# Kernel optimization log

Hardware: AMD Instinct MI355X
Metric: run time of the kernel (lower is better)

## Reference

```python
import jax, jax.numpy as jnp
import numpy as np

N = 10000
E = 640000
F = 128      # in_dim
H = 4        # heads
Dh = 32      # head_dim = ceil(128/4)
INNER = H * Dh   # 128 == out_dim -> W_out is Identity
OUT = 128
SCALE = 1.0 / np.sqrt(float(Dh))
LN_EPS = 1e-5


def setup_inputs() -> dict:
    key = jax.random.key(0)
    ks = jax.random.split(key, 8)
    s = 1.0 / np.sqrt(F)
    nodes = jax.random.normal(ks[0], (N, F), dtype=jnp.float32)
    edge_index = jax.random.randint(ks[1], (2, E), 0, N, dtype=jnp.int32)
    W_Q = jax.random.uniform(ks[2], (F, INNER), jnp.float32, -s, s)
    W_K = jax.random.uniform(ks[3], (F, INNER), jnp.float32, -s, s)
    W_V = jax.random.uniform(ks[4], (F, INNER), jnp.float32, -s, s)
    W_res = jax.random.uniform(ks[5], (F, OUT), jnp.float32, -s, s)
    b_res = jax.random.uniform(ks[6], (OUT,), jnp.float32, -s, s)
    gamma = jnp.ones((OUT,), jnp.float32)
    beta = jnp.zeros((OUT,), jnp.float32)
    return {"nodes": nodes, "W_Q": W_Q, "W_K": W_K, "W_V": W_V,
            "W_res": W_res, "b_res": b_res, "gamma": gamma, "beta": beta,
            "edge_index": edge_index}


def reference(nodes, W_Q, W_K, W_V, W_res, b_res, gamma, beta, edge_index):
    n = nodes.shape[0]
    src = edge_index[0]
    dst = edge_index[1]
    # node-level projections, split into heads: [N, H, Dh]
    Q = (nodes @ W_Q).reshape(n, H, Dh)
    K = (nodes @ W_K).reshape(n, H, Dh)
    V = (nodes @ W_V).reshape(n, H, Dh)
    # per-edge gathers: q from dst, k/v from src
    q = Q[dst]          # [E, H, Dh]
    k = K[src]
    v = V[src]
    score = jnp.sum(q * k, axis=-1) * SCALE      # [E, H]
    # segment softmax over dst
    mx = jax.ops.segment_max(score, dst, num_segments=n)   # [N, H]
    mx = jnp.where(jnp.isfinite(mx), mx, 0.0)               # guard empty segments
    ex = jnp.exp(score - mx[dst])                           # [E, H]
    sm = jax.ops.segment_sum(ex, dst, num_segments=n)       # [N, H]
    alpha = ex / (sm[dst] + 1e-12)                          # [E, H]
    # scatter-aggregate weighted values
    agg = jax.ops.segment_sum(alpha[:, :, None] * v, dst, num_segments=n)  # [N, H, Dh]
    H_cat = agg.reshape(n, INNER)                # W_out is Identity (inner == out)
    H_out = H_cat + nodes @ W_res + b_res        # residual projection
    # LayerNorm(out_dim)
    mu = jnp.mean(H_out, axis=-1, keepdims=True)
    var = jnp.mean(jnp.square(H_out - mu), axis=-1, keepdims=True)
    x_hat = (H_out - mu) * jax.lax.rsqrt(var + LN_EPS)
    return gamma * x_hat + beta
```

## Files before the change

kernel.cpp:

```cpp
#include <hip/hip_runtime.h>
#include <math.h>

#define FDIM 128
#define NP 64
#define NMAX 10240
static constexpr float SC2 = 0.17677669529663687f * 1.4426950408889634f;
static constexpr float LN_EPS = 1e-5f;

typedef __attribute__((ext_vector_type(8))) short bf16x8;
typedef __attribute__((ext_vector_type(4))) float f32x4;

__device__ __forceinline__ unsigned short f2bf(float f) {
    unsigned u = __float_as_uint(f);
    unsigned r = u + 0x7FFFu + ((u >> 16) & 1u);
    return (unsigned short)(r >> 16);
}

__global__ __launch_bounds__(256) void prep_kernel(
    const float* __restrict__ Wq, const float* __restrict__ Wk,
    const float* __restrict__ Wv, const float* __restrict__ Wr,
    unsigned short* __restrict__ Wt)
{
    const int tid = threadIdx.x;
    const int t = blockIdx.x;
    const int wiW = t >> 2, q = t & 3;
    const float* __restrict__ W = (wiW == 0) ? Wq : (wiW == 1) ? Wk : (wiW == 2) ? Wv : Wr;
    const int c = q * 32 + (tid >> 3);
    const int k0 = (tid & 7) * 16;
    unsigned short* dp = &Wt[(size_t)wiW * 16384 + c * 128 + k0];
    #pragma unroll
    for (int kk = 0; kk < 16; ++kk)
        dp[kk] = f2bf(W[(k0 + kk) * FDIM + c]);
}

__global__ __launch_bounds__(256) void gemm_hist_kernel(
    const float* __restrict__ nodes,
    const unsigned short* __restrict__ Wt,
    const float* __restrict__ br,
    unsigned short* __restrict__ Qu, unsigned short* __restrict__ KVu,
    float* __restrict__ Rb, int N,
    const int* __restrict__ dst, int* __restrict__ bh,
    int* __restrict__ rank, int E, int C)
{
    __shared__ __align__(16) char smem[52224];
    const int tid = threadIdx.x;
    const int wi = blockIdx.y;

    if (wi == 0) {
        const int p = blockIdx.x;
        if (p >= NP) return;
        int* h = (int*)smem;
        for (int i = tid; i < N; i += 256) h[i] = 0;
        __syncthreads();
        const int lo = p * C;
        const int hi = min(lo + C, E);
        const int n = hi - lo;
        if (n > 0) {
            if (((lo | E) & 3) == 0) {
                const int4* d4 = (const int4*)(dst + lo);
                int4* r4p = (int4*)(rank + lo);
                const int n4 = n >> 2;
                for (int i = tid; i < n4; i += 256) {
                    int4 d = d4[i];
                    int4 r;
                    r.x = atomicAdd(&h[d.x], 1);
                    r.y = atomicAdd(&h[d.y], 1);
                    r.z = atomicAdd(&h[d.z], 1);
                    r.w = atomicAdd(&h[d.w], 1);
                    r4p[i] = r;
                }
                for (int i = lo + (n4 << 2) + tid; i < hi; i += 256)
                    rank[i] = atomicAdd(&h[dst[i]], 1);
            } else {
                for (int i = lo + tid; i < hi; i += 256)
                    rank[i] = atomicAdd(&h[dst[i]], 1);
            }
        }
        __syncthreads();
        for (int i = tid; i < N; i += 256) bh[p * N + i] = h[i];
        return;
    }

    const int gw = wi - 1;
    const int row0 = blockIdx.x * 64;
    unsigned short (*As)[136] = (unsigned short(*)[136])smem;
    unsigned short (*Ws)[136] = (unsigned short(*)[136])(smem + 64 * 272);

    #pragma unroll
    for (int i = 0; i < 8; ++i) {
        const int idx = tid + i * 256;
        const int r = idx >> 5, c4 = idx & 31;
        const int gr = row0 + r;
        float4 v = make_float4(0.f, 0.f, 0.f, 0.f);
        if (gr < N) v = *reinterpret_cast<const float4*>(&nodes[(size_t)gr * FDIM + c4 * 4]);
        ushort4 o;
        o.x = f2bf(v.x); o.y = f2bf(v.y); o.z = f2bf(v.z); o.w = f2bf(v.w);
        *reinterpret_cast<ushort4*>(&As[r][c4 * 4]) = o;
    }
    const unsigned short* Wg = &Wt[(size_t)gw * 16384];
    #pragma unroll
    for (int i = 0; i < 8; ++i) {
        const int idx = tid + i * 256;
        const int r = idx >> 4, ch = idx & 15;
        const uint4 v = *reinterpret_cast<const uint4*>(&Wg[r * 128 + ch * 8]);
        *reinterpret_cast<uint4*>(&Ws[r][ch * 8]) = v;
    }
    __syncthreads();

    const int w = tid >> 6;
    const int l = tid & 63;
    const int lr = l & 15;
    const int lh = l >> 4;

    f32x4 acc[8];
    #pragma unroll
    for (int ct = 0; ct < 8; ++ct) acc[ct] = (f32x4){0.f, 0.f, 0.f, 0.f};

    #pragma unroll
    for (int kc = 0; kc < 4; ++kc) {
        const bf16x8 a = *reinterpret_cast<const bf16x8*>(&As[w * 16 + lr][kc * 32 + lh * 8]);
        #pragma unroll
        for (int ct = 0; ct < 8; ++ct) {
            const bf16x8 bb = *reinterpret_cast<const bf16x8*>(&Ws[ct * 16 + lr][kc * 32 + lh * 8]);
            acc[ct] = __builtin_amdgcn_mfma_f32_16x16x32_bf16(a, bb, acc[ct], 0, 0, 0);
        }
    }

    const int rbase = row0 + w * 16 + lh * 4;
    #pragma unroll
    for (int ct = 0; ct < 8; ++ct) {
        const int col = ct * 16 + lr;
        float bc = 0.f;
        if (gw == 3) bc = br[col];
        #pragma unroll
        for (int r = 0; r < 4; ++r) {
            const int row = rbase + r;
            if (row >= N) continue;
            const float val = acc[ct][r];
            if (gw == 0)      Qu[(size_t)row * 128 + col] = f2bf(val);
            else if (gw == 1) KVu[(size_t)row * 256 + col] = f2bf(val);
            else if (gw == 2) KVu[(size_t)row * 256 + 128 + col] = f2bf(val);
            else              Rb[(size_t)row * 128 + col] = val + bc;
        }
    }
}

__global__ __launch_bounds__(256) void deg_kernel(
    const int* __restrict__ bh, int* __restrict__ deg, int N)
{
    const int d = blockIdx.x * 256 + threadIdx.x;
    if (d < N) {
        int s = 0;
        #pragma unroll
        for (int p = 0; p < NP; ++p) s += bh[p * N + d];
        deg[d] = s;
    }
}

__global__ __launch_bounds__(1024) void scan_kernel(
    const int* __restrict__ deg, int* __restrict__ rowptr, int N)
{
    __shared__ int tot[NMAX];
    __shared__ int wsum[16];
    const int tid = threadIdx.x;
    const int lane = tid & 63;
    const int wid = tid >> 6;

    for (int d = tid; d < N; d += 1024) tot[d] = deg[d];
    __syncthreads();

    const int CH = (N + 1023) / 1024;
    const int b = tid * CH;
    const int e = min(b + CH, N);
    int s = 0;
    for (int i = b; i < e; ++i) s += tot[i];

    int incl = s;
    #pragma unroll
    for (int off = 1; off < 64; off <<= 1) {
        int t = __shfl_up(incl, off);
        if (lane >= off) incl += t;
    }
    if (lane == 63) wsum[wid] = incl;
    __syncthreads();
    if (wid == 0) {
        int v = (lane < 16) ? wsum[lane] : 0;
        #pragma unroll
        for (int off = 1; off < 16; off <<= 1) {
            int t = __shfl_up(v, off);
            if (lane >= off) v += t;
        }
        if (lane < 16) wsum[lane] = v;
    }
    __syncthreads();
    const int wbase = (wid > 0) ? wsum[wid - 1] : 0;
    int run = wbase + incl - s;
    for (int i = b; i < e; ++i) {
        const int t = tot[i];
        rowptr[i] = run;
        run += t;
    }
    if (tid == 1023) rowptr[N] = wsum[15];
}

__global__ __launch_bounds__(256) void base_kernel(
    int* __restrict__ bh, const int* __restrict__ rowptr, int N)
{
    const int d = blockIdx.x * 256 + threadIdx.x;
    if (d < N) {
        int c = rowptr[d];
        #pragma unroll
        for (int p = 0; p < NP; ++p) {
            const int cnt = bh[p * N + d];
            bh[p * N + d] = c;
            c += cnt;
        }
    }
}

__global__ __launch_bounds__(256) void scatter_kernel(
    const int* __restrict__ src, const int* __restrict__ dst,
    const int* __restrict__ rank, const int* __restrict__ base,
    int* __restrict__ ssrc, int N, int E, int C)
{
    const int p = blockIdx.x >> 3;
    const int sub = blockIdx.x & 7;
    const int CS = C >> 3;
    const int lo = p * C + sub * CS;
    const int hi = min(lo + CS, E);
    const int n = hi - lo;
    if (n <= 0) return;
    const int* bp = &base[p * N];

    if (((lo | E) & 3) == 0) {
        const int4* s4 = (const int4*)(src + lo);
        const int4* d4 = (const int4*)(dst + lo);
        const int4* r4 = (const int4*)(rank + lo);
        const int n4 = n >> 2;
        for (int i = threadIdx.x; i < n4; i += 256) {
            const int4 s = s4[i];
            const int4 d = d4[i];
            const int4 r = r4[i];
            ssrc[bp[d.x] + r.x] = s.x;
            ssrc[bp[d.y] + r.y] = s.y;
            ssrc[bp[d.z] + r.z] = s.z;
            ssrc[bp[d.w] + r.w] = s.w;
        }
        for (int i = lo + (n4 << 2) + threadIdx.x; i < hi; i += 256)
            ssrc[bp[dst[i]] + rank[i]] = src[i];
    } else {
        for (int i = lo + threadIdx.x; i < hi; i += 256)
            ssrc[bp[dst[i]] + rank[i]] = src[i];
    }
}

__global__ __launch_bounds__(256) void agg_kernel(
    const unsigned short* __restrict__ Qu, const unsigned short* __restrict__ KVu,
    const float* __restrict__ Rb,
    const int* __restrict__ rowptr, const int* __restrict__ ssrc,
    const float* __restrict__ gamma, const float* __restrict__ beta,
    float* __restrict__ out, int N)
{
    const int wave = threadIdx.x >> 6;
    const int lane = threadIdx.x & 63;
    const int qtr = lane >> 4;
    const int lq = lane & 15;
    const int n = blockIdx.x * 16 + wave * 4 + qtr;
    if (n >= N) return;
    const int d0 = lq * 8;

    const uint4 qu = *reinterpret_cast<const uint4*>(&Qu[(size_t)n * 128 + d0]);
    const float qf0 = __uint_as_float(qu.x << 16), qf1 = __uint_as_float(qu.x & 0xFFFF0000u);
    const float qf2 = __uint_as_float(qu.y << 16), qf3 = __uint_as_float(qu.y & 0xFFFF0000u);
    const float qf4 = __uint_as_float(qu.z << 16), qf5 = __uint_as_float(qu.z & 0xFFFF0000u);
    const float qf6 = __uint_as_float(qu.w << 16), qf7 = __uint_as_float(qu.w & 0xFFFF0000u);

    const int beg = rowptr[n];
    const int end = rowptr[n + 1];

    float4 A0a = make_float4(0.f, 0.f, 0.f, 0.f), A0b = A0a;
    float4 A1a = A0a, A1b = A0a, A2a = A0a, A2b = A0a, A3a = A0a, A3b = A0a;
    float L0 = 0.f, L1 = 0.f, L2 = 0.f, L3 = 0.f;

#define GATHER(S, NK, NV)                                                     \
    {                                                                         \
        const unsigned short* bp = &KVu[(size_t)(S) * 256 + d0];              \
        NK = *reinterpret_cast<const uint4*>(bp);                             \
        NV = *reinterpret_cast<const uint4*>(bp + 128);                       \
    }
#define STEP(KU, VU, Aa, Ab, L)                                               \
    {                                                                         \
        const float k0 = __uint_as_float((KU).x << 16), k1 = __uint_as_float((KU).x & 0xFFFF0000u); \
        const float k2 = __uint_as_float((KU).y << 16), k3 = __uint_as_float((KU).y & 0xFFFF0000u); \
        const float k4 = __uint_as_float((KU).z << 16), k5 = __uint_as_float((KU).z & 0xFFFF0000u); \
        const float k6 = __uint_as_float((KU).w << 16), k7 = __uint_as_float((KU).w & 0xFFFF0000u); \
        float p = qf0 * k0 + qf1 * k1 + qf2 * k2 + qf3 * k3                   \
                + qf4 * k4 + qf5 * k5 + qf6 * k6 + qf7 * k7;                  \
        p += __shfl_xor(p, 1);                                                \
        p += __shfl_xor(p, 2);                                                \
        const float e1 = exp2f(p * SC2);                                      \
        const float v0 = __uint_as_float((VU).x << 16), v1 = __uint_as_float((VU).x & 0xFFFF0000u); \
        const float v2 = __uint_as_float((VU).y << 16), v3 = __uint_as_float((VU).y & 0xFFFF0000u); \
        const float v4 = __uint_as_float((VU).z << 16), v5 = __uint_as_float((VU).z & 0xFFFF0000u); \
        const float v6 = __uint_as_float((VU).w << 16), v7 = __uint_as_float((VU).w & 0xFFFF0000u); \
        Aa.x += e1 * v0; Aa.y += e1 * v1; Aa.z += e1 * v2; Aa.w += e1 * v3;   \
        Ab.x += e1 * v4; Ab.y += e1 * v5; Ab.z += e1 * v6; Ab.w += e1 * v7;   \
        L += e1;                                                              \
    }

    uint4 nk0, nv0, nk1, nv1, nk2, nv2, nk3, nv3;
    int j = beg;
    const int nb = (end - beg) >> 2;
    if (nb > 0) {
        int c0i = ssrc[j], c1i = ssrc[j + 1], c2i = ssrc[j + 2], c3i = ssrc[j + 3];
        GATHER(c0i, nk0, nv0); GATHER(c1i, nk1, nv1);
        GATHER(c2i, nk2, nv2); GATHER(c3i, nk3, nv3);
        int x0 = ssrc[j + 4], x1 = ssrc[j + 5], x2 = ssrc[j + 6], x3 = ssrc[j + 7];
        for (int bi = 1; bi < nb; ++bi) {
            const uint4 ck0 = nk0, cv0 = nv0, ck1 = nk1, cv1 = nv1;
            const uint4 ck2 = nk2, cv2 = nv2, ck3 = nk3, cv3 = nv3;
            c0i = x0; c1i = x1; c2i = x2; c3i = x3;
            const int nbase = j + (bi + 1) * 4;
            x0 = ssrc[nbase]; x1 = ssrc[nbase + 1];
            x2 = ssrc[nbase + 2]; x3 = ssrc[nbase + 3];
            GATHER(c0i, nk0, nv0); GATHER(c1i, nk1, nv1);
            GATHER(c2i, nk2, nv2); GATHER(c3i, nk3, nv3);
            STEP(ck0, cv0, A0a, A0b, L0);
            STEP(ck1, cv1, A1a, A1b, L1);
            STEP(ck2, cv2, A2a, A2b, L2);
            STEP(ck3, cv3, A3a, A3b, L3);
        }
        STEP(nk0, nv0, A0a, A0b, L0);
        STEP(nk1, nv1, A1a, A1b, L1);
        STEP(nk2, nv2, A2a, A2b, L2);
        STEP(nk3, nv3, A3a, A3b, L3);
        j = beg + nb * 4;
    }
    for (; j < end; ++j) {
        const int s0 = ssrc[j];
        uint4 k0u, v0u;
        GATHER(s0, k0u, v0u);
        STEP(k0u, v0u, A0a, A0b, L0);
    }
#undef GATHER
#undef STEP

    const float L = (L0 + L1) + (L2 + L3);
    const float inv = 1.f / (L + 1e-12f);
    const float4 ra = *reinterpret_cast<const float4*>(&Rb[(size_t)n * 128 + d0]);
    const float4 rb = *reinterpret_cast<const float4*>(&Rb[(size_t)n * 128 + d0 + 4]);
    float xa0 = ((A0a.x + A1a.x) + (A2a.x + A3a.x)) * inv + ra.x;
    float xa1 = ((A0a.y + A1a.y) + (A2a.y + A3a.y)) * inv + ra.y;
    float xa2 = ((A0a.z + A1a.z) + (A2a.z + A3a.z)) * inv + ra.z;
    float xa3 = ((A0a.w + A1a.w) + (A2a.w + A3a.w)) * inv + ra.w;
    float xb0 = ((A0b.x + A1b.x) + (A2b.x + A3b.x)) * inv + rb.x;
    float xb1 = ((A0b.y + A1b.y) + (A2b.y + A3b.y)) * inv + rb.y;
    float xb2 = ((A0b.z + A1b.z) + (A2b.z + A3b.z)) * inv + rb.z;
    float xb3 = ((A0b.w + A1b.w) + (A2b.w + A3b.w)) * inv + rb.w;

    float s1v = (xa0 + xa1 + xa2 + xa3) + (xb0 + xb1 + xb2 + xb3);
    float s2v = xa0 * xa0 + xa1 * xa1 + xa2 * xa2 + xa3 * xa3
              + xb0 * xb0 + xb1 * xb1 + xb2 * xb2 + xb3 * xb3;
    #pragma unroll
    for (int off = 8; off; off >>= 1) {
        s1v += __shfl_xor(s1v, off);
        s2v += __shfl_xor(s2v, off);
    }
    const float mu = s1v * (1.f / 128.f);
    float var = s2v * (1.f / 128.f) - mu * mu;
    var = fmaxf(var, 0.f);
    const float rs = rsqrtf(var + LN_EPS);

    const float4 ga = *reinterpret_cast<const float4*>(&gamma[d0]);
    const float4 gb = *reinterpret_cast<const float4*>(&gamma[d0 + 4]);
    const float4 ba = *reinterpret_cast<const float4*>(&beta[d0]);
    const float4 bb = *reinterpret_cast<const float4*>(&beta[d0 + 4]);
    float4 oa, ob;
    oa.x = ga.x * (xa0 - mu) * rs + ba.x;
    oa.y = ga.y * (xa1 - mu) * rs + ba.y;
    oa.z = ga.z * (xa2 - mu) * rs + ba.z;
    oa.w = ga.w * (xa3 - mu) * rs + ba.w;
    ob.x = gb.x * (xb0 - mu) * rs + bb.x;
    ob.y = gb.y * (xb1 - mu) * rs + bb.y;
    ob.z = gb.z * (xb2 - mu) * rs + bb.z;
    ob.w = gb.w * (xb3 - mu) * rs + bb.w;
    *reinterpret_cast<float4*>(&out[(size_t)n * 128 + d0]) = oa;
    *reinterpret_cast<float4*>(&out[(size_t)n * 128 + d0 + 4]) = ob;
}

extern "C" void kernel_launch(void* const* d_in, const int* in_sizes, int n_in,
                              void* d_out, int out_size, void* d_ws, size_t ws_size,
                              hipStream_t stream)
{
    const float* nodes = (const float*)d_in[0];
    const float* W_Q   = (const float*)d_in[1];
    const float* W_K   = (const float*)d_in[2];
    const float* W_V   = (const float*)d_in[3];
    const float* W_res = (const float*)d_in[4];
    const float* b_res = (const float*)d_in[5];
    const float* gamma = (const float*)d_in[6];
    const float* beta  = (const float*)d_in[7];
    const int*   eidx  = (const int*)d_in[8];

    const int N = in_sizes[0] / FDIM;
    const int E = in_sizes[8] / 2;
    const int* src = eidx;
    const int* dst = eidx + E;

    float* out = (float*)d_out;

    unsigned short* KVu = (unsigned short*)d_ws;
    unsigned short* Qu  = KVu + (size_t)N * 256;
    unsigned short* Wt  = Qu + (size_t)N * 128;
    float* Rb   = (float*)(Wt + 4 * 16384);
    int* bh     = (int*)(Rb + (size_t)N * 128);
    int* rowptr = bh + (size_t)NP * N;
    int* deg    = rowptr + (N + 1);
    int* rank   = deg + N;
    int* ssrc   = rank + E;

    const int C = (((E + NP - 1) / NP) + 31) & ~31;
    const int nG = (N + 63) / 64;
    const int nB = (N + 255) / 256;

    prep_kernel<<<16, 256, 0, stream>>>(W_Q, W_K, W_V, W_res, Wt);

    dim3 ggrid(nG, 5);
    gemm_hist_kernel<<<ggrid, 256, 0, stream>>>(nodes, Wt, b_res,
                                                Qu, KVu, Rb, N, dst, bh, rank, E, C);
    deg_kernel<<<nB, 256, 0, stream>>>(bh, deg, N);
    scan_kernel<<<1, 1024, 0, stream>>>(deg, rowptr, N);
    base_kernel<<<nB, 256, 0, stream>>>(bh, rowptr, N);
    scatter_kernel<<<NP * 8, 256, 0, stream>>>(src, dst, rank, bh, ssrc, N, E, C);
    agg_kernel<<<(N + 15) / 16, 256, 0, stream>>>(Qu, KVu, Rb, rowptr, ssrc,
                                                  gamma, beta, out, N);
}
```

Baseline: 88.52 us.

## Fuse weight prep into GEMM, merge degree/base passes, triple-buffer agg gathers

Each GEMM block now transposes and converts the fp32 weights to bf16 in shared memory itself, so the separate prep kernel goes away. The per-partition offset computation moves into the degree kernel as relative offsets, and the scatter adds rowptr itself, so base_kernel and one launch are removed. The aggregation loop now keeps three groups of four edges in flight instead of one prefetched group, to hide gather latency. The cost is redundant weight conversion in every GEMM block, strided transposed LDS writes, and higher register pressure in agg_kernel.

Result: slower. 115.7 us (+30.7%).

```diff
diff --git a/kernel.cpp b/kernel.cpp
--- a/kernel.cpp
+++ b/kernel.cpp
@@ -16,26 +16,10 @@
     return (unsigned short)(r >> 16);
 }
 
-__global__ __launch_bounds__(256) void prep_kernel(
+__global__ __launch_bounds__(256) void gemm_hist_kernel(
+    const float* __restrict__ nodes,
     const float* __restrict__ Wq, const float* __restrict__ Wk,
     const float* __restrict__ Wv, const float* __restrict__ Wr,
-    unsigned short* __restrict__ Wt)
-{
-    const int tid = threadIdx.x;
-    const int t = blockIdx.x;
-    const int wiW = t >> 2, q = t & 3;
-    const float* __restrict__ W = (wiW == 0) ? Wq : (wiW == 1) ? Wk : (wiW == 2) ? Wv : Wr;
-    const int c = q * 32 + (tid >> 3);
-    const int k0 = (tid & 7) * 16;
-    unsigned short* dp = &Wt[(size_t)wiW * 16384 + c * 128 + k0];
-    #pragma unroll
-    for (int kk = 0; kk < 16; ++kk)
-        dp[kk] = f2bf(W[(k0 + kk) * FDIM + c]);
-}
-
-__global__ __launch_bounds__(256) void gemm_hist_kernel(
-    const float* __restrict__ nodes,
-    const unsigned short* __restrict__ Wt,
     const float* __restrict__ br,
     unsigned short* __restrict__ Qu, unsigned short* __restrict__ KVu,
     float* __restrict__ Rb, int N,
@@ -97,13 +81,17 @@
         o.x = f2bf(v.x); o.y = f2bf(v.y); o.z = f2bf(v.z); o.w = f2bf(v.w);
         *reinterpret_cast<ushort4*>(&As[r][c4 * 4]) = o;
     }
-    const unsigned short* Wg = &Wt[(size_t)gw * 16384];
-    #pragma unroll
-    for (int i = 0; i < 8; ++i) {
+    const float* __restrict__ Wg = (gw == 0) ? Wq : (gw == 1) ? Wk : (gw == 2) ? Wv : Wr;
+    #pragma unroll
+    for (int i = 0; i < 16; ++i) {
         const int idx = tid + i * 256;
-        const int r = idx >> 4, ch = idx & 15;
-        const uint4 v = *reinterpret_cast<const uint4*>(&Wg[r * 128 + ch * 8]);
-        *reinterpret_cast<uint4*>(&Ws[r][ch * 8]) = v;
+        const int kr = idx >> 5;
+        const int c0i = (idx & 31) * 4;
+        const float4 v = *reinterpret_cast<const float4*>(&Wg[kr * FDIM + c0i]);
+        Ws[c0i + 0][kr] = f2bf(v.x);
+        Ws[c0i + 1][kr] = f2bf(v.y);
+        Ws[c0i + 2][kr] = f2bf(v.z);
+        Ws[c0i + 3][kr] = f2bf(v.w);
     }
     __syncthreads();
 
@@ -145,15 +133,19 @@
     }
 }
 
-__global__ __launch_bounds__(256) void deg_kernel(
-    const int* __restrict__ bh, int* __restrict__ deg, int N)
+__global__ __launch_bounds__(256) void degrel_kernel(
+    int* __restrict__ bh, int* __restrict__ deg, int N)
 {
     const int d = blockIdx.x * 256 + threadIdx.x;
     if (d < N) {
-        int s = 0;
+        int c = 0;
         #pragma unroll
-        for (int p = 0; p < NP; ++p) s += bh[p * N + d];
-        deg[d] = s;
+        for (int p = 0; p < NP; ++p) {
+            const int cnt = bh[p * N + d];
+            bh[p * N + d] = c;
+            c += cnt;
+        }
+        deg[d] = c;
     }
 }
 
@@ -203,25 +195,11 @@
     if (tid == 1023) rowptr[N] = wsum[15];
 }
 
-__global__ __launch_bounds__(256) void base_kernel(
-    int* __restrict__ bh, const int* __restrict__ rowptr, int N)
-{
-    const int d = blockIdx.x * 256 + threadIdx.x;
-    if (d < N) {
-        int c = rowptr[d];
-        #pragma unroll
-        for (int p = 0; p < NP; ++p) {
-            const int cnt = bh[p * N + d];
-            bh[p * N + d] = c;
-            c += cnt;
-        }
-    }
-}
-
 __global__ __launch_bounds__(256) void scatter_kernel(
     const int* __restrict__ src, const int* __restrict__ dst,
-    const int* __restrict__ rank, const int* __restrict__ base,
-    int* __restrict__ ssrc, int N, int E, int C)
+    const int* __restrict__ rank, const int* __restrict__ rel,
+    const int* __restrict__ rowptr, int* __restrict__ ssrc,
+    int N, int E, int C)
 {
     const int p = blockIdx.x >> 3;
     const int sub = blockIdx.x & 7;
@@ -230,7 +208,7 @@
     const int hi = min(lo + CS, E);
     const int n = hi - lo;
     if (n <= 0) return;
-    const int* bp = &base[p * N];
+    const int* rp = &rel[p * N];
 
     if (((lo | E) & 3) == 0) {
         const int4* s4 = (const int4*)(src + lo);
@@ -241,16 +219,16 @@
             const int4 s = s4[i];
             const int4 d = d4[i];
             const int4 r = r4[i];
-            ssrc[bp[d.x] + r.x] = s.x;
-            ssrc[bp[d.y] + r.y] = s.y;
-            ssrc[bp[d.z] + r.z] = s.z;
-            ssrc[bp[d.w] + r.w] = s.w;
+            ssrc[rowptr[d.x] + rp[d.x] + r.x] = s.x;
+            ssrc[rowptr[d.y] + rp[d.y] + r.y] = s.y;
+            ssrc[rowptr[d.z] + rp[d.z] + r.z] = s.z;
+            ssrc[rowptr[d.w] + rp[d.w] + r.w] = s.w;
         }
         for (int i = lo + (n4 << 2) + threadIdx.x; i < hi; i += 256)
-            ssrc[bp[dst[i]] + rank[i]] = src[i];
+            ssrc[rowptr[dst[i]] + rp[dst[i]] + rank[i]] = src[i];
     } else {
         for (int i = lo + threadIdx.x; i < hi; i += 256)
-            ssrc[bp[dst[i]] + rank[i]] = src[i];
+            ssrc[rowptr[dst[i]] + rp[dst[i]] + rank[i]] = src[i];
     }
 }
 
@@ -282,12 +260,6 @@
     float4 A1a = A0a, A1b = A0a, A2a = A0a, A2b = A0a, A3a = A0a, A3b = A0a;
     float L0 = 0.f, L1 = 0.f, L2 = 0.f, L3 = 0.f;
 
-#define GATHER(S, NK, NV)                                                     \
-    {                                                                         \
-        const unsigned short* bp = &KVu[(size_t)(S) * 256 + d0];              \
-        NK = *reinterpret_cast<const uint4*>(bp);                             \
-        NV = *reinterpret_cast<const uint4*>(bp + 128);                       \
-    }
 #define STEP(KU, VU, Aa, Ab, L)                                               \
     {                                                                         \
         const float k0 = __uint_as_float((KU).x << 16), k1 = __uint_as_float((KU).x & 0xFFFF0000u); \
@@ -307,42 +279,67 @@
         Ab.x += e1 * v4; Ab.y += e1 * v5; Ab.z += e1 * v6; Ab.w += e1 * v7;   \
         L += e1;                                                              \
     }
-
-    uint4 nk0, nv0, nk1, nv1, nk2, nv2, nk3, nv3;
+#define GATH(P, JJ)                                                           \
+    {                                                                         \
+        const int t0 = ssrc[JJ], t1 = ssrc[(JJ) + 1];                         \
+        const int t2 = ssrc[(JJ) + 2], t3 = ssrc[(JJ) + 3];                   \
+        const unsigned short* p0 = &KVu[(size_t)t0 * 256 + d0];               \
+        const unsigned short* p1 = &KVu[(size_t)t1 * 256 + d0];               \
+        const unsigned short* p2 = &KVu[(size_t)t2 * 256 + d0];               \
+        const unsigned short* p3 = &KVu[(size_t)t3 * 256 + d0];               \
+        P##K0 = *reinterpret_cast<const uint4*>(p0);                          \
+        P##V0 = *reinterpret_cast<const uint4*>(p0 + 128);                    \
+        P##K1 = *reinterpret_cast<const uint4*>(p1);                          \
+        P##V1 = *reinterpret_cast<const uint4*>(p1 + 128);                    \
+        P##K2 = *reinterpret_cast<const uint4*>(p2);                          \
+        P##V2 = *reinterpret_cast<const uint4*>(p2 + 128);                    \
+        P##K3 = *reinterpret_cast<const uint4*>(p3);                          \
+        P##V3 = *reinterpret_cast<const uint4*>(p3 + 128);                    \
+    }
+#define STEP4(P)                                                              \
+    STEP(P##K0, P##V0, A0a, A0b, L0);                                         \
+    STEP(P##K1, P##V1, A1a, A1b, L1);                                         \
+    STEP(P##K2, P##V2, A2a, A2b, L2);                                         \
+    STEP(P##K3, P##V3, A3a, A3b, L3);
+
+    uint4 aK0, aV0, aK1, aV1, aK2, aV2, aK3, aV3;
+    uint4 bK0, bV0, bK1, bV1, bK2, bV2, bK3, bV3;
+    uint4 cK0, cV0, cK1, cV1, cK2, cV2, cK3, cV3;
+
     int j = beg;
     const int nb = (end - beg) >> 2;
-    if (nb > 0) {
-        int c0i = ssrc[j], c1i = ssrc[j + 1], c2i = ssrc[j + 2], c3i = ssrc[j + 3];
-        GATHER(c0i, nk0, nv0); GATHER(c1i, nk1, nv1);
-        GATHER(c2i, nk2, nv2); GATHER(c3i, nk3, nv3);
-        int x0 = ssrc[j + 4], x1 = ssrc[j + 5], x2 = ssrc[j + 6], x3 = ssrc[j + 7];
-        for (int bi = 1; bi < nb; ++bi) {
-            const uint4 ck0 = nk0, cv0 = nv0, ck1 = nk1, cv1 = nv1;
-            const uint4 ck2 = nk2, cv2 = nv2, ck3 = nk3, cv3 = nv3;
-            c0i = x0; c1i = x1; c2i = x2; c3i = x3;
-            const int nbase = j + (bi + 1) * 4;
-            x0 = ssrc[nbase]; x1 = ssrc[nbase + 1];
-            x2 = ssrc[nbase + 2]; x3 = ssrc[nbase + 3];
-            GATHER(c0i, nk0, nv0); GATHER(c1i, nk1, nv1);
-            GATHER(c2i, nk2, nv2); GATHER(c3i, nk3, nv3);
-            STEP(ck0, cv0, A0a, A0b, L0);
-            STEP(ck1, cv1, A1a, A1b, L1);
-            STEP(ck2, cv2, A2a, A2b, L2);
-            STEP(ck3, cv3, A3a, A3b, L3);
-        }
-        STEP(nk0, nv0, A0a, A0b, L0);
-        STEP(nk1, nv1, A1a, A1b, L1);
-        STEP(nk2, nv2, A2a, A2b, L2);
-        STEP(nk3, nv3, A3a, A3b, L3);
+    if (nb >= 3) {
+        GATH(a, j); GATH(b, j + 4); GATH(c, j + 8);
+        int bi = 0;
+        for (; bi + 5 < nb; bi += 3) {
+            STEP4(a); GATH(a, j + (bi + 3) * 4);
+            STEP4(b); GATH(b, j + (bi + 4) * 4);
+            STEP4(c); GATH(c, j + (bi + 5) * 4);
+        }
+        STEP4(a);
+        if (bi + 3 < nb) GATH(a, j + (bi + 3) * 4);
+        STEP4(b);
+        if (bi + 4 < nb) GATH(b, j + (bi + 4) * 4);
+        STEP4(c);
+        if (bi + 3 < nb) { STEP4(a); }
+        if (bi + 4 < nb) { STEP4(b); }
+        j = beg + nb * 4;
+    } else if (nb > 0) {
+        GATH(a, j);
+        if (nb == 2) GATH(b, j + 4);
+        STEP4(a);
+        if (nb == 2) { STEP4(b); }
         j = beg + nb * 4;
     }
     for (; j < end; ++j) {
         const int s0 = ssrc[j];
-        uint4 k0u, v0u;
-        GATHER(s0, k0u, v0u);
+        const unsigned short* bp = &KVu[(size_t)s0 * 256 + d0];
+        const uint4 k0u = *reinterpret_cast<const uint4*>(bp);
+        const uint4 v0u = *reinterpret_cast<const uint4*>(bp + 128);
         STEP(k0u, v0u, A0a, A0b, L0);
     }
-#undef GATHER
+#undef STEP4
+#undef GATH
 #undef STEP
 
     const float L = (L0 + L1) + (L2 + L3);
@@ -411,8 +408,7 @@
 
     unsigned short* KVu = (unsigned short*)d_ws;
     unsigned short* Qu  = KVu + (size_t)N * 256;
-    unsigned short* Wt  = Qu + (size_t)N * 128;
-    float* Rb   = (float*)(Wt + 4 * 16384);
+    float* Rb   = (float*)(Qu + (size_t)N * 128);
     int* bh     = (int*)(Rb + (size_t)N * 128);
     int* rowptr = bh + (size_t)NP * N;
     int* deg    = rowptr + (N + 1);
@@ -423,15 +419,12 @@
     const int nG = (N + 63) / 64;
     const int nB = (N + 255) / 256;
 
-    prep_kernel<<<16, 256, 0, stream>>>(W_Q, W_K, W_V, W_res, Wt);
-
     dim3 ggrid(nG, 5);
-    gemm_hist_kernel<<<ggrid, 256, 0, stream>>>(nodes, Wt, b_res,
+    gemm_hist_kernel<<<ggrid, 256, 0, stream>>>(nodes, W_Q, W_K, W_V, W_res, b_res,
                                                 Qu, KVu, Rb, N, dst, bh, rank, E, C);
-    deg_kernel<<<nB, 256, 0, stream>>>(bh, deg, N);
+    degrel_kernel<<<nB, 256, 0, stream>>>(bh, deg, N);
     scan_kernel<<<1, 1024, 0, stream>>>(deg, rowptr, N);
-    base_kernel<<<nB, 256, 0, stream>>>(bh, rowptr, N);
-    scatter_kernel<<<NP * 8, 256, 0, stream>>>(src, dst, rank, bh, ssrc, N, E, C);
+    scatter_kernel<<<NP * 8, 256, 0, stream>>>(src, dst, rank, bh, rowptr, ssrc, N, E, C);
     agg_kernel<<<(N + 15) / 16, 256, 0, stream>>>(Qu, KVu, Rb, rowptr, ssrc,
                                                   gamma, beta, out, N);
 }
```

## Fold weight prep into GEMM and merge base offsets into degree pass

Applied to the files above, without the earlier changes.

Drops the separate weight-transpose/bf16 prep kernel: each GEMM block now reads fp32 weights directly, converts them to bf16 and transposes them into shared memory. It also folds the per-partition base computation into the degree kernel as relative offsets, so the scatter adds rowptr at write time and the base kernel launch goes away. This removes two launches and one full pass over the histogram. In exchange, every GEMM block does redundant weight conversion with scattered 2-byte LDS stores, and the scatter does an extra rowptr gather per edge.

Result: slower. 95.80 us (+8.2%).

```diff
diff --git a/kernel.cpp b/kernel.cpp
--- a/kernel.cpp
+++ b/kernel.cpp
@@ -16,26 +16,10 @@
     return (unsigned short)(r >> 16);
 }
 
-__global__ __launch_bounds__(256) void prep_kernel(
+__global__ __launch_bounds__(256) void gemm_hist_kernel(
+    const float* __restrict__ nodes,
     const float* __restrict__ Wq, const float* __restrict__ Wk,
     const float* __restrict__ Wv, const float* __restrict__ Wr,
-    unsigned short* __restrict__ Wt)
-{
-    const int tid = threadIdx.x;
-    const int t = blockIdx.x;
-    const int wiW = t >> 2, q = t & 3;
-    const float* __restrict__ W = (wiW == 0) ? Wq : (wiW == 1) ? Wk : (wiW == 2) ? Wv : Wr;
-    const int c = q * 32 + (tid >> 3);
-    const int k0 = (tid & 7) * 16;
-    unsigned short* dp = &Wt[(size_t)wiW * 16384 + c * 128 + k0];
-    #pragma unroll
-    for (int kk = 0; kk < 16; ++kk)
-        dp[kk] = f2bf(W[(k0 + kk) * FDIM + c]);
-}
-
-__global__ __launch_bounds__(256) void gemm_hist_kernel(
-    const float* __restrict__ nodes,
-    const unsigned short* __restrict__ Wt,
     const float* __restrict__ br,
     unsigned short* __restrict__ Qu, unsigned short* __restrict__ KVu,
     float* __restrict__ Rb, int N,
@@ -97,13 +81,17 @@
         o.x = f2bf(v.x); o.y = f2bf(v.y); o.z = f2bf(v.z); o.w = f2bf(v.w);
         *reinterpret_cast<ushort4*>(&As[r][c4 * 4]) = o;
     }
-    const unsigned short* Wg = &Wt[(size_t)gw * 16384];
-    #pragma unroll
-    for (int i = 0; i < 8; ++i) {
+    const float* __restrict__ Wg = (gw == 0) ? Wq : (gw == 1) ? Wk : (gw == 2) ? Wv : Wr;
+    #pragma unroll
+    for (int i = 0; i < 16; ++i) {
         const int idx = tid + i * 256;
-        const int r = idx >> 4, ch = idx & 15;
-        const uint4 v = *reinterpret_cast<const uint4*>(&Wg[r * 128 + ch * 8]);
-        *reinterpret_cast<uint4*>(&Ws[r][ch * 8]) = v;
+        const int kr = idx >> 5;
+        const int c0i = (idx & 31) * 4;
+        const float4 v = *reinterpret_cast<const float4*>(&Wg[kr * FDIM + c0i]);
+        Ws[c0i + 0][kr] = f2bf(v.x);
+        Ws[c0i + 1][kr] = f2bf(v.y);
+        Ws[c0i + 2][kr] = f2bf(v.z);
+        Ws[c0i + 3][kr] = f2bf(v.w);
     }
     __syncthreads();
 
@@ -145,15 +133,19 @@
     }
 }
 
-__global__ __launch_bounds__(256) void deg_kernel(
-    const int* __restrict__ bh, int* __restrict__ deg, int N)
+__global__ __launch_bounds__(256) void degrel_kernel(
+    int* __restrict__ bh, int* __restrict__ deg, int N)
 {
     const int d = blockIdx.x * 256 + threadIdx.x;
     if (d < N) {
-        int s = 0;
+        int c = 0;
         #pragma unroll
-        for (int p = 0; p < NP; ++p) s += bh[p * N + d];
-        deg[d] = s;
+        for (int p = 0; p < NP; ++p) {
+            const int cnt = bh[p * N + d];
+            bh[p * N + d] = c;
+            c += cnt;
+        }
+        deg[d] = c;
     }
 }
 
@@ -203,25 +195,11 @@
     if (tid == 1023) rowptr[N] = wsum[15];
 }
 
-__global__ __launch_bounds__(256) void base_kernel(
-    int* __restrict__ bh, const int* __restrict__ rowptr, int N)
-{
-    const int d = blockIdx.x * 256 + threadIdx.x;
-    if (d < N) {
-        int c = rowptr[d];
-        #pragma unroll
-        for (int p = 0; p < NP; ++p) {
-            const int cnt = bh[p * N + d];
-            bh[p * N + d] = c;
-            c += cnt;
-        }
-    }
-}
-
 __global__ __launch_bounds__(256) void scatter_kernel(
     const int* __restrict__ src, const int* __restrict__ dst,
-    const int* __restrict__ rank, const int* __restrict__ base,
-    int* __restrict__ ssrc, int N, int E, int C)
+    const int* __restrict__ rank, const int* __restrict__ rel,
+    const int* __restrict__ rowptr, int* __restrict__ ssrc,
+    int N, int E, int C)
 {
     const int p = blockIdx.x >> 3;
     const int sub = blockIdx.x & 7;
@@ -230,7 +208,7 @@
     const int hi = min(lo + CS, E);
     const int n = hi - lo;
     if (n <= 0) return;
-    const int* bp = &base[p * N];
+    const int* rp = &rel[p * N];
 
     if (((lo | E) & 3) == 0) {
         const int4* s4 = (const int4*)(src + lo);
@@ -241,16 +219,16 @@
             const int4 s = s4[i];
             const int4 d = d4[i];
             const int4 r = r4[i];
-            ssrc[bp[d.x] + r.x] = s.x;
-            ssrc[bp[d.y] + r.y] = s.y;
-            ssrc[bp[d.z] + r.z] = s.z;
-            ssrc[bp[d.w] + r.w] = s.w;
+            ssrc[rowptr[d.x] + rp[d.x] + r.x] = s.x;
+            ssrc[rowptr[d.y] + rp[d.y] + r.y] = s.y;
+            ssrc[rowptr[d.z] + rp[d.z] + r.z] = s.z;
+            ssrc[rowptr[d.w] + rp[d.w] + r.w] = s.w;
         }
         for (int i = lo + (n4 << 2) + threadIdx.x; i < hi; i += 256)
-            ssrc[bp[dst[i]] + rank[i]] = src[i];
+            ssrc[rowptr[dst[i]] + rp[dst[i]] + rank[i]] = src[i];
     } else {
         for (int i = lo + threadIdx.x; i < hi; i += 256)
-            ssrc[bp[dst[i]] + rank[i]] = src[i];
+            ssrc[rowptr[dst[i]] + rp[dst[i]] + rank[i]] = src[i];
     }
 }
 
@@ -411,8 +389,7 @@
 
     unsigned short* KVu = (unsigned short*)d_ws;
     unsigned short* Qu  = KVu + (size_t)N * 256;
-    unsigned short* Wt  = Qu + (size_t)N * 128;
-    float* Rb   = (float*)(Wt + 4 * 16384);
+    float* Rb   = (float*)(Qu + (size_t)N * 128);
     int* bh     = (int*)(Rb + (size_t)N * 128);
     int* rowptr = bh + (size_t)NP * N;
     int* deg    = rowptr + (N + 1);
@@ -423,15 +400,12 @@
     const int nG = (N + 63) / 64;
     const int nB = (N + 255) / 256;
 
-    prep_kernel<<<16, 256, 0, stream>>>(W_Q, W_K, W_V, W_res, Wt);
-
     dim3 ggrid(nG, 5);
-    gemm_hist_kernel<<<ggrid, 256, 0, stream>>>(nodes, Wt, b_res,
+    gemm_hist_kernel<<<ggrid, 256, 0, stream>>>(nodes, W_Q, W_K, W_V, W_res, b_res,
                                                 Qu, KVu, Rb, N, dst, bh, rank, E, C);
-    deg_kernel<<<nB, 256, 0, stream>>>(bh, deg, N);
+    degrel_kernel<<<nB, 256, 0, stream>>>(bh, deg, N);
     scan_kernel<<<1, 1024, 0, stream>>>(deg, rowptr, N);
-    base_kernel<<<nB, 256, 0, stream>>>(bh, rowptr, N);
-    scatter_kernel<<<NP * 8, 256, 0, stream>>>(src, dst, rank, bh, ssrc, N, E, C);
+    scatter_kernel<<<NP * 8, 256, 0, stream>>>(src, dst, rank, bh, rowptr, ssrc, N, E, C);
     agg_kernel<<<(N + 15) / 16, 256, 0, stream>>>(Qu, KVu, Rb, rowptr, ssrc,
                                                   gamma, beta, out, N);
 }
```
